# Optimization experiments

Hardware: AMD Instinct MI355X
Metric: run time of the kernel (lower is better)

Reference implementation:

```python
import jax, jax.numpy as jnp
import numpy as np

DIM = 1024
QK_DIM = 128
HIDDEN = 2048  # int(2.0 * DIM)
B, N = 4, 4096


def setup_inputs() -> dict:
    key = jax.random.key(0)
    ks = jax.random.split(key, 10)
    std = 0.02
    return {
        "x": jax.random.normal(ks[0], (B, N, DIM), dtype=jnp.float32),
        "ln_g": jnp.ones((DIM,), jnp.float32),
        "ln_b": jnp.zeros((DIM,), jnp.float32),
        "W_hidden": jax.random.normal(ks[1], (DIM, 2 * HIDDEN), jnp.float32) * (1.0 / np.sqrt(DIM)),
        "b_hidden": jnp.zeros((2 * HIDDEN,), jnp.float32),
        "W_qk": jax.random.normal(ks[2], (DIM, QK_DIM), jnp.float32) * (1.0 / np.sqrt(DIM)),
        "b_qk": jnp.zeros((QK_DIM,), jnp.float32),
        "os_gamma": jax.random.normal(ks[3], (2, QK_DIM), jnp.float32) * std,
        "os_beta": jnp.zeros((2, QK_DIM), jnp.float32),
        "W_out": jax.random.normal(ks[4], (HIDDEN, DIM), jnp.float32) * (1.0 / np.sqrt(HIDDEN)),
        "b_out": jnp.zeros((DIM,), jnp.float32),
    }


def _layernorm(x, g, b, eps=1e-5):
    mu = jnp.mean(x, axis=-1, keepdims=True)
    var = jnp.var(x, axis=-1, keepdims=True)
    return (x - mu) * jax.lax.rsqrt(var + eps) * g + b


def reference(x, ln_g, ln_b, W_hidden, b_hidden, W_qk, b_qk, os_gamma, os_beta, W_out, b_out):
    n = x.shape[-2]
    normed = _layernorm(x, ln_g, ln_b)
    hidden = jax.nn.silu(normed @ W_hidden + b_hidden)  # [b,n,2*hidden]
    v, gate = jnp.split(hidden, 2, axis=-1)             # [b,n,hidden] each
    qk = jax.nn.silu(normed @ W_qk + b_qk)              # [b,n,qk]
    q = qk * os_gamma[0] + os_beta[0]
    k = qk * os_gamma[1] + os_beta[1]
    sim = jnp.einsum('bid,bjd->bij', q, k)
    # causal: divide row i by (i+1)
    denom = (jnp.arange(n, dtype=x.dtype) + 1.0)[:, None]  # [n,1]
    sim = sim / denom
    attn = jnp.square(jax.nn.relu(sim))
    causal_mask = jnp.triu(jnp.ones((n, n), dtype=bool), k=1)
    attn = jnp.where(causal_mask, 0.0, attn)
    out = jnp.einsum('bij,bjd->bid', attn, v)
    out = out * gate
    out = out @ W_out + b_out
    return out + x
```

## Files before the change

### kernel.cpp

```cpp
#include <hip/hip_runtime.h>
#include <hip/hip_bf16.h>
#include <stdint.h>

typedef __bf16 bf16_t;
typedef __bf16 bf16x4 __attribute__((ext_vector_type(4)));
typedef __bf16 bf16x8 __attribute__((ext_vector_type(8)));
typedef float  f32x4  __attribute__((ext_vector_type(4)));
typedef long long i64;

#define MFMA16(a, b, c) __builtin_amdgcn_mfma_f32_16x16x32_bf16((a), (b), (c), 0, 0, 0)
#define MFMAF8(a, b, c) __builtin_amdgcn_mfma_f32_16x16x32_fp8_fp8((a), (b), (c), 0, 0, 0)

static constexpr int TOKS   = 16384;
static constexpr int SEQ    = 4096;
static constexpr int DIMK   = 1024;
static constexpr int H2     = 4096;
static constexpr int HID    = 2048;
static constexpr int QKD    = 128;
static constexpr int SMEM8P = 131072;
static constexpr size_t PBATCH = 8912896;

__device__ __forceinline__ void gload_lds16b(const uint8_t* g, uint8_t* l) {
  __builtin_amdgcn_global_load_lds((__attribute__((address_space(1))) void*)(g),
                                   (__attribute__((address_space(3))) void*)(l),
                                   16, 0, 0);
}

__device__ __forceinline__ float silu_f(float v) { return v / (1.0f + __expf(-v)); }

__device__ __forceinline__ uint32_t f8x4(float a, float b, float c, float d) {
  int v = __builtin_amdgcn_cvt_pk_fp8_f32(a, b, 0, false);
  v = __builtin_amdgcn_cvt_pk_fp8_f32(c, d, v, true);
  return (uint32_t)v;
}
__device__ __forceinline__ uint8_t f8x1(float a) {
  return (uint8_t)(__builtin_amdgcn_cvt_pk_fp8_f32(a, 0.f, 0, false) & 0xff);
}

#define BARRIER() __builtin_amdgcn_s_barrier()

__global__ __launch_bounds__(256) void k_transpose_bf16(const float* __restrict__ W,
                                                        bf16_t* __restrict__ WT,
                                                        int K, int N) {
  __shared__ float t[32][33];
  int n0 = blockIdx.x * 32, k0 = blockIdx.y * 32;
  int tx = threadIdx.x & 31, ty = threadIdx.x >> 5;
#pragma unroll
  for (int r = 0; r < 32; r += 8)
    t[ty + r][tx] = W[(size_t)(k0 + ty + r) * N + n0 + tx];
  __syncthreads();
#pragma unroll
  for (int r = 0; r < 32; r += 8)
    WT[(size_t)(n0 + ty + r) * K + k0 + tx] = (bf16_t)t[tx][ty + r];
}

__global__ __launch_bounds__(256) void k_transpose_f8(const float* __restrict__ W,
                                                      uint8_t* __restrict__ WT,
                                                      int K, int N) {
  __shared__ float t[32][33];
  int n0 = blockIdx.x * 32, k0 = blockIdx.y * 32;
  int tx = threadIdx.x & 31, ty = threadIdx.x >> 5;
#pragma unroll
  for (int r = 0; r < 32; r += 8)
    t[ty + r][tx] = W[(size_t)(k0 + ty + r) * N + n0 + tx];
  __syncthreads();
#pragma unroll
  for (int r = 0; r < 32; r += 8)
    WT[(size_t)(n0 + ty + r) * K + k0 + tx] = f8x1(t[tx][ty + r] * 16.0f);
}

__global__ __launch_bounds__(256) void k_layernorm(const float* __restrict__ x,
                                                   const float* __restrict__ g,
                                                   const float* __restrict__ b,
                                                   bf16_t* __restrict__ out,
                                                   uint8_t* __restrict__ out8) {
  int row = blockIdx.x, t = threadIdx.x;
  const float4* xr = (const float4*)(x + (size_t)row * DIMK);
  float4 v = xr[t];
  float s  = v.x + v.y + v.z + v.w;
  float ss = v.x * v.x + v.y * v.y + v.z * v.z + v.w * v.w;
#pragma unroll
  for (int o = 1; o < 64; o <<= 1) { s += __shfl_xor(s, o); ss += __shfl_xor(ss, o); }
  __shared__ float red[8];
  int wave = t >> 6, lane = t & 63;
  if (lane == 0) { red[wave] = s; red[wave + 4] = ss; }
  __syncthreads();
  s  = red[0] + red[1] + red[2] + red[3];
  ss = red[4] + red[5] + red[6] + red[7];
  float mean = s * (1.0f / DIMK);
  float var  = ss * (1.0f / DIMK) - mean * mean;
  float rstd = rsqrtf(var + 1e-5f);
  float4 gg = ((const float4*)g)[t];
  float4 bb = ((const float4*)b)[t];
  float o0 = (v.x - mean) * rstd * gg.x + bb.x;
  float o1 = (v.y - mean) * rstd * gg.y + bb.y;
  float o2 = (v.z - mean) * rstd * gg.z + bb.z;
  float o3 = (v.w - mean) * rstd * gg.w + bb.w;
  bf16x4 o4; o4[0] = (bf16_t)o0; o4[1] = (bf16_t)o1; o4[2] = (bf16_t)o2; o4[3] = (bf16_t)o3;
  *(bf16x4*)(out + (size_t)row * DIMK + t * 4) = o4;
  *(uint32_t*)(out8 + (size_t)row * DIMK + t * 4) = f8x4(o0, o1, o2, o3);
}

#define MFMAQ8(MH, KP)                                                        \
  _Pragma("unroll")                                                           \
  for (int mi = 0; mi < 4; ++mi)                                              \
    _Pragma("unroll")                                                         \
    for (int nj = 0; nj < 4; ++nj)                                            \
      _Pragma("unroll")                                                       \
      for (int ks = 0; ks < 2; ++ks)                                          \
        acc[(MH) * 4 + mi][nj] = MFMAF8(aF[(MH) * 4 + mi][KP][ks],            \
                                        bF[nj][KP][ks], acc[(MH) * 4 + mi][nj]);

#define RDA8(MILO, KP, BUFO)                                                  \
  _Pragma("unroll")                                                           \
  for (int mi = (MILO); mi < (MILO) + 4; ++mi)                                \
    _Pragma("unroll")                                                         \
    for (int ks = 0; ks < 2; ++ks)                                            \
      aF[mi][KP][ks] = *(const i64*)(pA + (BUFO) + mi * 2048 + swzK[(KP) * 2 + ks]);

#define RDB8(KP, BUFO)                                                        \
  _Pragma("unroll")                                                           \
  for (int nj = 0; nj < 4; ++nj)                                              \
    _Pragma("unroll")                                                         \
    for (int ks = 0; ks < 2; ++ks)                                            \
      bF[nj][KP][ks] = *(const i64*)(pB + (BUFO) + nj * 2048 + swzK[(KP) * 2 + ks]);

__device__ __forceinline__ void core8p_f8(const uint8_t* __restrict__ Ag, int lda,
                                          const uint8_t* __restrict__ Bg, int ldb,
                                          int NK, uint8_t* AS, uint8_t* BS,
                                          f32x4 (&acc)[8][4]) {
  const int tid = threadIdx.x, wid = tid >> 6, lane = tid & 63;
  const int wm = wid >> 2, wn = wid & 3;

  auto stA = [&](int kt, int h) {
    int r0 = h * 128 + wid * 16 + (lane >> 3);
    int c0 = ((lane & 7) ^ ((r0 >> 1) & 7)) * 16;
    uint8_t* d = AS + ((kt & 1) * 2 + h) * 16384 + wid * 2048;
    gload_lds16b(Ag + (size_t)r0 * lda + kt * 128 + c0, d);
    int r1 = r0 + 8;
    int c1 = ((lane & 7) ^ ((r1 >> 1) & 7)) * 16;
    gload_lds16b(Ag + (size_t)r1 * lda + kt * 128 + c1, d + 1024);
  };
  auto stB = [&](int kt, int h) {
    int r0 = h * 128 + wid * 16 + (lane >> 3);
    int c0 = ((lane & 7) ^ ((r0 >> 1) & 7)) * 16;
    uint8_t* d = BS + ((kt & 1) * 2 + h) * 16384 + wid * 2048;
    gload_lds16b(Bg + (size_t)r0 * ldb + kt * 128 + c0, d);
    int r1 = r0 + 8;
    int c1 = ((lane & 7) ^ ((r1 >> 1) & 7)) * 16;
    gload_lds16b(Bg + (size_t)r1 * ldb + kt * 128 + c1, d + 1024);
  };

  int swzK[4];
#pragma unroll
  for (int j = 0; j < 4; ++j)
    swzK[j] = ((j * 4 + (lane >> 4)) ^ (lane & 14)) * 8;

  const uint8_t* pA = AS + wm * 16384 + (lane & 15) * 128;
  const uint8_t* pB = BS + (wn >> 1) * 16384 + ((wn & 1) * 64 + (lane & 15)) * 128;

  i64 aF[8][2][2], bF[4][2][2];

  stA(0, 0); stA(0, 1); stB(0, 0); stB(0, 1);
  stB(1, 0); stB(1, 1);
  asm volatile("s_waitcnt vmcnt(4)" ::: "memory");
  BARRIER();
  RDA8(0, 0, 0);
  RDB8(0, 0);

  for (int g = 0; g < NK; ++g) {
    const int buf  = (g & 1) * 32768;
    const int nbuf = ((g + 1) & 1) * 32768;
    RDA8(4, 0, buf);
    if (g + 1 < NK) stA(g + 1, 0);
    BARRIER();
    __builtin_amdgcn_s_setprio(1);
    MFMAQ8(0, 0);
    __builtin_amdgcn_s_setprio(0);
    RDA8(0, 1, buf);
    RDB8(1, buf);
    if (g + 1 < NK) stA(g + 1, 1);
    BARRIER();
    __builtin_amdgcn_s_setprio(1);
    MFMAQ8(1, 0);
    __builtin_amdgcn_s_setprio(0);
    RDA8(4, 1, buf);
    BARRIER();
    __builtin_amdgcn_s_setprio(1);
    MFMAQ8(0, 1);
    __builtin_amdgcn_s_setprio(0);
    if (g + 2 < NK) {
      stB(g + 2, 0); stB(g + 2, 1);
      asm volatile("s_waitcnt vmcnt(4)" ::: "memory");
    } else if (g + 1 < NK) {
      asm volatile("s_waitcnt vmcnt(0)" ::: "memory");
    }
    BARRIER();
    if (g + 1 < NK) {
      RDA8(0, 0, nbuf);
      RDB8(0, nbuf);
    }
    __builtin_amdgcn_s_setprio(1);
    MFMAQ8(1, 1);
    __builtin_amdgcn_s_setprio(0);
  }
}

__global__ __launch_bounds__(512, 2) void k_gemm_hidden8p(const uint8_t* __restrict__ A,
                                                          const uint8_t* __restrict__ BT,
                                                          const float* __restrict__ bias,
                                                          uint8_t* __restrict__ vT8,
                                                          bf16_t* __restrict__ gate) {
  extern __shared__ __align__(16) uint8_t lds[];
  uint8_t* AS = lds;
  uint8_t* BS = lds + 65536;
  const int nwg = gridDim.x, bid = blockIdx.x;
  const int swz = (bid & 7) * (nwg >> 3) + (bid >> 3);
  const int mblk = swz >> 4, nblk = swz & 15;
  const int m0 = mblk * 256, n0 = nblk * 256;
  f32x4 acc[8][4];
#pragma unroll
  for (int i = 0; i < 8; ++i)
#pragma unroll
    for (int j = 0; j < 4; ++j) acc[i][j] = (f32x4){0.f, 0.f, 0.f, 0.f};
  core8p_f8(A + (size_t)m0 * DIMK, DIMK, BT + (size_t)n0 * DIMK, DIMK,
            DIMK / 128, AS, BS, acc);

  const int tid = threadIdx.x, wid = tid >> 6, lane = tid & 63;
  const int wm = wid >> 2, wn = wid & 3;
  const int row0 = m0 + wm * 128, col0 = n0 + wn * 64;
#pragma unroll
  for (int mi = 0; mi < 8; ++mi)
#pragma unroll
    for (int nj = 0; nj < 4; ++nj) {
      int col = col0 + nj * 16 + (lane & 15);
      float bv = bias[col];
      int row = row0 + mi * 16 + ((lane >> 4) << 2);
      float sv[4];
#pragma unroll
      for (int r = 0; r < 4; ++r) sv[r] = silu_f(acc[mi][nj][r] * 0.0625f + bv);
      if (col < HID) {
        *(uint32_t*)(vT8 + (size_t)col * TOKS + row) =
            f8x4(sv[0] * 16.f, sv[1] * 16.f, sv[2] * 16.f, sv[3] * 16.f);
      } else {
#pragma unroll
        for (int r = 0; r < 4; ++r)
          gate[(size_t)(row + r) * HID + (col - HID)] = (bf16_t)sv[r];
      }
    }
}

__global__ __launch_bounds__(512, 2) void k_gemm_out8p(const uint8_t* __restrict__ A,
                                                       const uint8_t* __restrict__ BT,
                                                       const float* __restrict__ bo,
                                                       const float* __restrict__ x,
                                                       float* __restrict__ out) {
  extern __shared__ __align__(16) uint8_t lds[];
  uint8_t* AS = lds;
  uint8_t* BS = lds + 65536;
  const int nwg = gridDim.x, bid = blockIdx.x;
  const int swz = (bid & 7) * (nwg >> 3) + (bid >> 3);
  const int mblk = swz >> 2, nblk = swz & 3;
  const int m0 = mblk * 256, n0 = nblk * 256;
  f32x4 acc[8][4];
#pragma unroll
  for (int i = 0; i < 8; ++i)
#pragma unroll
    for (int j = 0; j < 4; ++j) acc[i][j] = (f32x4){0.f, 0.f, 0.f, 0.f};
  core8p_f8(A + (size_t)m0 * HID, HID, BT + (size_t)n0 * HID, HID,
            HID / 128, AS, BS, acc);

  const int tid = threadIdx.x, wid = tid >> 6, lane = tid & 63;
  const int wm = wid >> 2, wn = wid & 3;
  const int row0 = m0 + wm * 128, col0 = n0 + wn * 64;
#pragma unroll
  for (int mi = 0; mi < 8; ++mi)
#pragma unroll
    for (int nj = 0; nj < 4; ++nj) {
      int col = col0 + nj * 16 + (lane & 15);
      float bv = bo[col];
      int row = row0 + mi * 16 + ((lane >> 4) << 2);
#pragma unroll
      for (int r = 0; r < 4; ++r) {
        size_t gi = (size_t)(row + r) * DIMK + col;
        out[gi] = acc[mi][nj][r] * (1.0f / 4096.0f) + bv + x[gi];
      }
    }
}

__global__ __launch_bounds__(512, 2) void k_pv8p(const uint8_t* __restrict__ P8,
                                                 const uint8_t* __restrict__ vT8,
                                                 const bf16_t* __restrict__ gate,
                                                 uint8_t* __restrict__ gated8) {
  extern __shared__ __align__(16) uint8_t lds[];
  uint8_t* AS = lds;
  uint8_t* BS = lds + 65536;
  const int w = blockIdx.x;
  const int rb = 15 - (w >> 5);
  const int hb = (w >> 2) & 7;
  const int bb = w & 3;
  const int lda = (rb + 1) * 256;
  const uint8_t* Ag = P8 + (size_t)bb * PBATCH + (size_t)65536 * (rb * (rb + 1) / 2);
  const uint8_t* Bg = vT8 + (size_t)(hb * 256) * TOKS + (size_t)bb * SEQ;
  f32x4 acc[8][4];
#pragma unroll
  for (int i = 0; i < 8; ++i)
#pragma unroll
    for (int j = 0; j < 4; ++j) acc[i][j] = (f32x4){0.f, 0.f, 0.f, 0.f};
  core8p_f8(Ag, lda, Bg, TOKS, (rb + 1) * 2, AS, BS, acc);

  const int tid = threadIdx.x, wid = tid >> 6, lane = tid & 63;
  const int wm = wid >> 2, wn = wid & 3;
  const int row0 = rb * 256 + wm * 128, col0 = hb * 256 + wn * 64;
#pragma unroll
  for (int mi = 0; mi < 8; ++mi)
#pragma unroll
    for (int nj = 0; nj < 4; ++nj) {
      int col = col0 + nj * 16 + (lane & 15);
      int row = row0 + mi * 16 + ((lane >> 4) << 2);
#pragma unroll
      for (int r = 0; r < 4; ++r) {
        size_t gi = (size_t)(bb * SEQ + row + r) * HID + col;
        float gv = (float)gate[gi];
        gated8[gi] = f8x1(acc[mi][nj][r] * gv * 6.103515625e-05f);
      }
    }
}

__device__ __forceinline__ void gload_lds16(const bf16_t* g, bf16_t* l) {
  __builtin_amdgcn_global_load_lds((__attribute__((address_space(1))) void*)(g),
                                   (__attribute__((address_space(3))) void*)(l),
                                   16, 0, 0);
}

__device__ __forceinline__ void gemm_core_std(const bf16_t* __restrict__ Ag0, int lda,
                                              const bf16_t* __restrict__ Bg0, int ldb,
                                              int K, bf16_t* As, bf16_t* Bs,
                                              f32x4 acc[4][4]) {
  const int tid = threadIdx.x;
  const int wave = tid >> 6, lane = tid & 63;
  bf16_t* asw = As + wave * 32 * 32;
  bf16_t* bsw = Bs + wave * 32 * 32;
  const int ar = ((wave >> 1) * 64 + (lane & 15)) * 32 + (lane >> 4) * 8;
  const int br = ((wave & 1) * 64 + (lane & 15)) * 32 + (lane >> 4) * 8;
  for (int k0 = 0; k0 < K; k0 += 32) {
    __syncthreads();
    gload_lds16(Ag0 + k0, asw);
    gload_lds16(Ag0 + k0 + 16 * lda, asw + 16 * 32);
    gload_lds16(Bg0 + k0, bsw);
    gload_lds16(Bg0 + k0 + 16 * ldb, bsw + 16 * 32);
    __syncthreads();
    bf16x8 af[4], bfr[4];
#pragma unroll
    for (int m = 0; m < 4; m++) af[m] = *(const bf16x8*)(As + ar + m * 16 * 32);
#pragma unroll
    for (int n = 0; n < 4; n++) bfr[n] = *(const bf16x8*)(Bs + br + n * 16 * 32);
#pragma unroll
    for (int m = 0; m < 4; m++)
#pragma unroll
      for (int n = 0; n < 4; n++) acc[m][n] = MFMA16(af[m], bfr[n], acc[m][n]);
  }
}

__global__ __launch_bounds__(256) void k_gemm_qk(const bf16_t* __restrict__ A,
                                                 const bf16_t* __restrict__ BT,
                                                 const float* __restrict__ bias,
                                                 const float* __restrict__ osg,
                                                 const float* __restrict__ osb,
                                                 bf16_t* __restrict__ qo,
                                                 bf16_t* __restrict__ ko) {
  __shared__ __align__(16) bf16_t As[128 * 32];
  __shared__ __align__(16) bf16_t Bs[128 * 32];
  const int tid = threadIdx.x, wave = tid >> 6, lane = tid & 63;
  const int m0 = blockIdx.y * 128;
  const bf16_t* Ag0 = A + (size_t)(m0 + wave * 32 + (lane >> 2)) * DIMK + (lane & 3) * 8;
  const bf16_t* Bg0 = BT + (size_t)(wave * 32 + (lane >> 2)) * DIMK + (lane & 3) * 8;
  f32x4 acc[4][4];
#pragma unroll
  for (int m = 0; m < 4; m++)
#pragma unroll
    for (int n = 0; n < 4; n++) acc[m][n] = (f32x4){0.f, 0.f, 0.f, 0.f};
  gemm_core_std(Ag0, DIMK, Bg0, DIMK, DIMK, As, Bs, acc);

  const int row0 = m0 + (wave >> 1) * 64;
  const int col0 = (wave & 1) * 64;
#pragma unroll
  for (int m = 0; m < 4; m++) {
#pragma unroll
    for (int n = 0; n < 4; n++) {
      int col = col0 + n * 16 + (lane & 15);
      float bv = bias[col];
      float g0 = osg[col], b0 = osb[col];
      float g1 = osg[QKD + col], b1 = osb[QKD + col];
      int row = row0 + m * 16 + ((lane >> 4) << 2);
#pragma unroll
      for (int r = 0; r < 4; r++) {
        float sv = silu_f(acc[m][n][r] + bv);
        qo[(size_t)(row + r) * QKD + col] = (bf16_t)(sv * g0 + b0);
        ko[(size_t)(row + r) * QKD + col] = (bf16_t)(sv * g1 + b1);
      }
    }
  }
}

__global__ __launch_bounds__(256) void k_qkt(const bf16_t* __restrict__ qb,
                                             const bf16_t* __restrict__ kb,
                                             uint8_t* __restrict__ P8) {
  const int jb = blockIdx.x, ib = blockIdx.y, bb = blockIdx.z;
  const int rb = ib >> 1;
  if (jb > 2 * rb + 1) return;
  const int lda = (rb + 1) * 256;
  uint8_t* Pt = P8 + (size_t)bb * PBATCH + (size_t)65536 * (rb * (rb + 1) / 2)
              + (size_t)((ib & 1) * 128) * lda + jb * 128;
  if (jb == ib + 1) {
    const int row = threadIdx.x >> 1, cb = (threadIdx.x & 1) * 64;
    uint4 z = {0, 0, 0, 0};
#pragma unroll
    for (int c = 0; c < 64; c += 16)
      *(uint4*)(Pt + (size_t)row * lda + cb + c) = z;
    return;
  }
  __shared__ __align__(16) bf16_t As[128 * 32];
  __shared__ __align__(16) bf16_t Bs[128 * 32];
  const int tid = threadIdx.x, wave = tid >> 6, lane = tid & 63;
  const bf16_t* Ag0 = qb + (size_t)(bb * SEQ + ib * 128 + wave * 32 + (lane >> 2)) * QKD + (lane & 3) * 8;
  const bf16_t* Bg0 = kb + (size_t)(bb * SEQ + jb * 128 + wave * 32 + (lane >> 2)) * QKD + (lane & 3) * 8;
  f32x4 acc[4][4];
#pragma unroll
  for (int m = 0; m < 4; m++)
#pragma unroll
    for (int n = 0; n < 4; n++) acc[m][n] = (f32x4){0.f, 0.f, 0.f, 0.f};
  gemm_core_std(Ag0, QKD, Bg0, QKD, QKD, As, Bs, acc);

  const int il0 = (wave >> 1) * 64, jl0 = (wave & 1) * 64;
#pragma unroll
  for (int m = 0; m < 4; m++) {
#pragma unroll
    for (int n = 0; n < 4; n++) {
      int jloc = jl0 + n * 16 + (lane & 15);
      int jg = jb * 128 + jloc;
#pragma unroll
      for (int r = 0; r < 4; r++) {
        int iloc = il0 + m * 16 + ((lane >> 4) << 2) + r;
        int ig = ib * 128 + iloc;
        float sv = acc[m][n][r] / (float)(ig + 1);
        sv = fmaxf(sv, 0.f);
        sv *= sv;
        if (jg > ig) sv = 0.f;
        Pt[(size_t)iloc * lda + jloc] = f8x1(sv * 262144.0f);
      }
    }
  }
}

extern "C" void kernel_launch(void* const* d_in, const int* in_sizes, int n_in,
                              void* d_out, int out_size, void* d_ws, size_t ws_size,
                              hipStream_t stream) {
  (void)in_sizes; (void)n_in; (void)out_size; (void)ws_size;
  const float* x    = (const float*)d_in[0];
  const float* ln_g = (const float*)d_in[1];
  const float* ln_b = (const float*)d_in[2];
  const float* Wh   = (const float*)d_in[3];
  const float* bh   = (const float*)d_in[4];
  const float* Wqk  = (const float*)d_in[5];
  const float* bqk  = (const float*)d_in[6];
  const float* osg  = (const float*)d_in[7];
  const float* osb  = (const float*)d_in[8];
  const float* Wo   = (const float*)d_in[9];
  const float* bo   = (const float*)d_in[10];
  float* out = (float*)d_out;

  char* ws = (char*)d_ws;
  bf16_t* normed  = (bf16_t*)ws;  ws += (size_t)TOKS * DIMK * 2;
  uint8_t* normed8 = (uint8_t*)ws; ws += (size_t)TOKS * DIMK;
  bf16_t* WqkT    = (bf16_t*)ws;  ws += (size_t)QKD * DIMK * 2;
  uint8_t* Wh8T   = (uint8_t*)ws; ws += (size_t)H2 * DIMK;
  uint8_t* Wo8T   = (uint8_t*)ws; ws += (size_t)DIMK * HID;
  bf16_t* gate    = (bf16_t*)ws;  ws += (size_t)TOKS * HID * 2;
  uint8_t* vT8    = (uint8_t*)ws; ws += (size_t)HID * TOKS;
  uint8_t* gated8 = (uint8_t*)ws; ws += (size_t)TOKS * HID;
  bf16_t* qb      = (bf16_t*)ws;  ws += (size_t)TOKS * QKD * 2;
  bf16_t* kb      = (bf16_t*)ws;  ws += (size_t)TOKS * QKD * 2;
  uint8_t* P8     = (uint8_t*)ws; ws += (size_t)4 * PBATCH;

  hipFuncSetAttribute((const void*)k_gemm_hidden8p,
                      hipFuncAttributeMaxDynamicSharedMemorySize, SMEM8P);
  hipFuncSetAttribute((const void*)k_gemm_out8p,
                      hipFuncAttributeMaxDynamicSharedMemorySize, SMEM8P);
  hipFuncSetAttribute((const void*)k_pv8p,
                      hipFuncAttributeMaxDynamicSharedMemorySize, SMEM8P);

  k_transpose_f8<<<dim3(H2 / 32, DIMK / 32), 256, 0, stream>>>(Wh, Wh8T, DIMK, H2);
  k_transpose_f8<<<dim3(DIMK / 32, HID / 32), 256, 0, stream>>>(Wo, Wo8T, HID, DIMK);
  k_transpose_bf16<<<dim3(QKD / 32, DIMK / 32), 256, 0, stream>>>(Wqk, WqkT, DIMK, QKD);
  k_layernorm<<<TOKS, 256, 0, stream>>>(x, ln_g, ln_b, normed, normed8);
  k_gemm_hidden8p<<<dim3((TOKS / 256) * (H2 / 256)), 512, SMEM8P, stream>>>(normed8, Wh8T, bh, vT8, gate);
  k_gemm_qk<<<dim3(1, TOKS / 128), 256, 0, stream>>>(normed, WqkT, bqk, osg, osb, qb, kb);
  k_qkt<<<dim3(SEQ / 128, SEQ / 128, 4), 256, 0, stream>>>(qb, kb, P8);
  k_pv8p<<<dim3(16 * 8 * 4), 512, SMEM8P, stream>>>(P8, vT8, gate, gated8);
  k_gemm_out8p<<<dim3((TOKS / 256) * (DIMK / 256)), 512, SMEM8P, stream>>>(gated8, Wo8T, bo, x, out);
}
```

Before: 406.8 us.

## Switch FP8 GEMM core to scaled 16x16x128 MFMA with new LDS swizzle

Replaces the four 16x16x32 fp8 MFMAs per K-tile slice with the gfx950 scaled 16x16x128 f8f6f4 MFMA using unit scales. Fragments are now read from LDS as two 16-byte loads per lane, and the swizzle pattern changes to match. The register layout and read schedule are restructured to fit, which cuts the MFMA instruction count and LDS read instructions. It risks K-ordering and layout mismatches between the operands, and a different register pressure profile.

```diff
diff --git a/kernel.cpp b/kernel.cpp
--- a/kernel.cpp
+++ b/kernel.cpp
@@ -6,10 +6,11 @@
 typedef __bf16 bf16x4 __attribute__((ext_vector_type(4)));
 typedef __bf16 bf16x8 __attribute__((ext_vector_type(8)));
 typedef float  f32x4  __attribute__((ext_vector_type(4)));
-typedef long long i64;
+typedef int    i32x8  __attribute__((ext_vector_type(8)));
 
 #define MFMA16(a, b, c) __builtin_amdgcn_mfma_f32_16x16x32_bf16((a), (b), (c), 0, 0, 0)
-#define MFMAF8(a, b, c) __builtin_amdgcn_mfma_f32_16x16x32_fp8_fp8((a), (b), (c), 0, 0, 0)
+#define MFMAMX(a, b, c) \
+  __builtin_amdgcn_mfma_scale_f32_16x16x128_f8f6f4((a), (b), (c), 0, 0, 0, 127, 0, 127)
 
 static constexpr int TOKS   = 16384;
 static constexpr int SEQ    = 4096;
@@ -35,6 +36,12 @@
 }
 __device__ __forceinline__ uint8_t f8x1(float a) {
   return (uint8_t)(__builtin_amdgcn_cvt_pk_fp8_f32(a, 0.f, 0, false) & 0xff);
+}
+
+__device__ __forceinline__ i32x8 rd32(const uint8_t* p0, const uint8_t* p1) {
+  const int4 lo = *(const int4*)p0;
+  const int4 hi = *(const int4*)p1;
+  return (i32x8){lo.x, lo.y, lo.z, lo.w, hi.x, hi.y, hi.z, hi.w};
 }
 
 #define BARRIER() __builtin_amdgcn_s_barrier()
@@ -101,29 +108,22 @@
   *(uint32_t*)(out8 + (size_t)row * DIMK + t * 4) = f8x4(o0, o1, o2, o3);
 }
 
-#define MFMAQ8(MH, KP)                                                        \
+#define RDAF(MILO, BUFO)                                                      \
   _Pragma("unroll")                                                           \
-  for (int mi = 0; mi < 4; ++mi)                                              \
+  for (int mi = (MILO); mi < (MILO) + 2; ++mi)                                \
+    aF[mi] = rd32(pA + (BUFO) + mi * 2048 + sw0, pA + (BUFO) + mi * 2048 + sw1);
+
+#define RDBF(BUFO)                                                            \
+  _Pragma("unroll")                                                           \
+  for (int nj = 0; nj < 4; ++nj)                                              \
+    bF[nj] = rd32(pB + (BUFO) + nj * 2048 + sw0, pB + (BUFO) + nj * 2048 + sw1);
+
+#define MFMAQX(Q)                                                             \
+  _Pragma("unroll")                                                           \
+  for (int mi = (Q) * 2; mi < (Q) * 2 + 2; ++mi)                              \
     _Pragma("unroll")                                                         \
     for (int nj = 0; nj < 4; ++nj)                                            \
-      _Pragma("unroll")                                                       \
-      for (int ks = 0; ks < 2; ++ks)                                          \
-        acc[(MH) * 4 + mi][nj] = MFMAF8(aF[(MH) * 4 + mi][KP][ks],            \
-                                        bF[nj][KP][ks], acc[(MH) * 4 + mi][nj]);
-
-#define RDA8(MILO, KP, BUFO)                                                  \
-  _Pragma("unroll")                                                           \
-  for (int mi = (MILO); mi < (MILO) + 4; ++mi)                                \
-    _Pragma("unroll")                                                         \
-    for (int ks = 0; ks < 2; ++ks)                                            \
-      aF[mi][KP][ks] = *(const i64*)(pA + (BUFO) + mi * 2048 + swzK[(KP) * 2 + ks]);
-
-#define RDB8(KP, BUFO)                                                        \
-  _Pragma("unroll")                                                           \
-  for (int nj = 0; nj < 4; ++nj)                                              \
-    _Pragma("unroll")                                                         \
-    for (int ks = 0; ks < 2; ++ks)                                            \
-      bF[nj][KP][ks] = *(const i64*)(pB + (BUFO) + nj * 2048 + swzK[(KP) * 2 + ks]);
+      acc[mi][nj] = MFMAMX(aF[mi], bF[nj], acc[mi][nj]);
 
 __device__ __forceinline__ void core8p_f8(const uint8_t* __restrict__ Ag, int lda,
                                           const uint8_t* __restrict__ Bg, int ldb,
@@ -134,60 +134,54 @@
 
   auto stA = [&](int kt, int h) {
     int r0 = h * 128 + wid * 16 + (lane >> 3);
-    int c0 = ((lane & 7) ^ ((r0 >> 1) & 7)) * 16;
+    int c0 = ((lane & 7) ^ ((lane >> 3) & 7)) * 16;
     uint8_t* d = AS + ((kt & 1) * 2 + h) * 16384 + wid * 2048;
     gload_lds16b(Ag + (size_t)r0 * lda + kt * 128 + c0, d);
-    int r1 = r0 + 8;
-    int c1 = ((lane & 7) ^ ((r1 >> 1) & 7)) * 16;
-    gload_lds16b(Ag + (size_t)r1 * lda + kt * 128 + c1, d + 1024);
+    gload_lds16b(Ag + (size_t)(r0 + 8) * lda + kt * 128 + c0, d + 1024);
   };
   auto stB = [&](int kt, int h) {
     int r0 = h * 128 + wid * 16 + (lane >> 3);
-    int c0 = ((lane & 7) ^ ((r0 >> 1) & 7)) * 16;
+    int c0 = ((lane & 7) ^ ((lane >> 3) & 7)) * 16;
     uint8_t* d = BS + ((kt & 1) * 2 + h) * 16384 + wid * 2048;
     gload_lds16b(Bg + (size_t)r0 * ldb + kt * 128 + c0, d);
-    int r1 = r0 + 8;
-    int c1 = ((lane & 7) ^ ((r1 >> 1) & 7)) * 16;
-    gload_lds16b(Bg + (size_t)r1 * ldb + kt * 128 + c1, d + 1024);
+    gload_lds16b(Bg + (size_t)(r0 + 8) * ldb + kt * 128 + c0, d + 1024);
   };
 
-  int swzK[4];
-#pragma unroll
-  for (int j = 0; j < 4; ++j)
-    swzK[j] = ((j * 4 + (lane >> 4)) ^ (lane & 14)) * 8;
+  const int t = lane >> 4;
+  const int sw0 = ((2 * t) ^ (lane & 7)) * 16;
+  const int sw1 = ((2 * t + 1) ^ (lane & 7)) * 16;
 
   const uint8_t* pA = AS + wm * 16384 + (lane & 15) * 128;
   const uint8_t* pB = BS + (wn >> 1) * 16384 + ((wn & 1) * 64 + (lane & 15)) * 128;
 
-  i64 aF[8][2][2], bF[4][2][2];
+  i32x8 aF[8], bF[4];
 
   stA(0, 0); stA(0, 1); stB(0, 0); stB(0, 1);
   stB(1, 0); stB(1, 1);
   asm volatile("s_waitcnt vmcnt(4)" ::: "memory");
   BARRIER();
-  RDA8(0, 0, 0);
-  RDB8(0, 0);
+  RDAF(0, 0);
+  RDBF(0);
 
   for (int g = 0; g < NK; ++g) {
     const int buf  = (g & 1) * 32768;
     const int nbuf = ((g + 1) & 1) * 32768;
-    RDA8(4, 0, buf);
+    RDAF(2, buf);
     if (g + 1 < NK) stA(g + 1, 0);
     BARRIER();
     __builtin_amdgcn_s_setprio(1);
-    MFMAQ8(0, 0);
+    MFMAQX(0);
     __builtin_amdgcn_s_setprio(0);
-    RDA8(0, 1, buf);
-    RDB8(1, buf);
+    RDAF(4, buf);
     if (g + 1 < NK) stA(g + 1, 1);
     BARRIER();
     __builtin_amdgcn_s_setprio(1);
-    MFMAQ8(1, 0);
+    MFMAQX(1);
     __builtin_amdgcn_s_setprio(0);
-    RDA8(4, 1, buf);
+    RDAF(6, buf);
     BARRIER();
     __builtin_amdgcn_s_setprio(1);
-    MFMAQ8(0, 1);
+    MFMAQX(2);
     __builtin_amdgcn_s_setprio(0);
     if (g + 2 < NK) {
       stB(g + 2, 0); stB(g + 2, 1);
@@ -197,11 +191,11 @@
     }
     BARRIER();
     if (g + 1 < NK) {
-      RDA8(0, 0, nbuf);
-      RDB8(0, nbuf);
+      RDAF(0, nbuf);
+      RDBF(nbuf);
     }
     __builtin_amdgcn_s_setprio(1);
-    MFMAQ8(1, 1);
+    MFMAQX(3);
     __builtin_amdgcn_s_setprio(0);
   }
 }
```

Result: slower. 1.455 ms (+257.6%).

## Permute fp8 K-dimension layout so MFMA operands load as 128-bit LDS reads

Applied to the files above, without the earlier changes.

All fp8 producers (weight transpose, layernorm, vT, gated, P) now write each 128-wide K chunk in a permuted order. In that order, the two 8-byte fragments a lane needs for consecutive MFMA k-steps sit next to each other. The fp8 GEMM core then reads each fragment pair with one 16-byte LDS load instead of two 8-byte loads, and the row-dependent swizzle is simplified. This halves the number of LDS read instructions in the core, at the cost of scattered byte-level stores in the epilogues and more index arithmetic.

```diff
diff --git a/kernel.cpp b/kernel.cpp
--- a/kernel.cpp
+++ b/kernel.cpp
@@ -7,6 +7,7 @@
 typedef __bf16 bf16x8 __attribute__((ext_vector_type(8)));
 typedef float  f32x4  __attribute__((ext_vector_type(4)));
 typedef long long i64;
+typedef long long i64x2 __attribute__((ext_vector_type(2)));
 
 #define MFMA16(a, b, c) __builtin_amdgcn_mfma_f32_16x16x32_bf16((a), (b), (c), 0, 0, 0)
 #define MFMAF8(a, b, c) __builtin_amdgcn_mfma_f32_16x16x32_fp8_fp8((a), (b), (c), 0, 0, 0)
@@ -37,6 +38,11 @@
   return (uint8_t)(__builtin_amdgcn_cvt_pk_fp8_f32(a, 0.f, 0, false) & 0xff);
 }
 
+__device__ __forceinline__ int permk(int kb) {
+  int b = kb & 7, t = (kb >> 3) & 3, s = (kb >> 5) & 1, a = (kb >> 6) & 1;
+  return (a << 6) | (t << 4) | (s << 3) | b;
+}
+
 #define BARRIER() __builtin_amdgcn_s_barrier()
 
 __global__ __launch_bounds__(256) void k_transpose_bf16(const float* __restrict__ W,
@@ -65,8 +71,11 @@
     t[ty + r][tx] = W[(size_t)(k0 + ty + r) * N + n0 + tx];
   __syncthreads();
 #pragma unroll
-  for (int r = 0; r < 32; r += 8)
-    WT[(size_t)(n0 + ty + r) * K + k0 + tx] = f8x1(t[tx][ty + r] * 16.0f);
+  for (int r = 0; r < 32; r += 8) {
+    int kt = k0 + tx;
+    WT[(size_t)(n0 + ty + r) * K + (kt & ~127) + permk(kt & 127)] =
+        f8x1(t[tx][ty + r] * 16.0f);
+  }
 }
 
 __global__ __launch_bounds__(256) void k_layernorm(const float* __restrict__ x,
@@ -98,7 +107,9 @@
   float o3 = (v.w - mean) * rstd * gg.w + bb.w;
   bf16x4 o4; o4[0] = (bf16_t)o0; o4[1] = (bf16_t)o1; o4[2] = (bf16_t)o2; o4[3] = (bf16_t)o3;
   *(bf16x4*)(out + (size_t)row * DIMK + t * 4) = o4;
-  *(uint32_t*)(out8 + (size_t)row * DIMK + t * 4) = f8x4(o0, o1, o2, o3);
+  int kt = t * 4;
+  *(uint32_t*)(out8 + (size_t)row * DIMK + (kt & ~127) + permk(kt & 127)) =
+      f8x4(o0, o1, o2, o3);
 }
 
 #define MFMAQ8(MH, KP)                                                        \
@@ -114,16 +125,12 @@
 #define RDA8(MILO, KP, BUFO)                                                  \
   _Pragma("unroll")                                                           \
   for (int mi = (MILO); mi < (MILO) + 4; ++mi)                                \
-    _Pragma("unroll")                                                         \
-    for (int ks = 0; ks < 2; ++ks)                                            \
-      aF[mi][KP][ks] = *(const i64*)(pA + (BUFO) + mi * 2048 + swzK[(KP) * 2 + ks]);
+    aF[mi][KP] = *(const i64x2*)(pA + (BUFO) + mi * 2048 + swc[KP]);
 
 #define RDB8(KP, BUFO)                                                        \
   _Pragma("unroll")                                                           \
   for (int nj = 0; nj < 4; ++nj)                                              \
-    _Pragma("unroll")                                                         \
-    for (int ks = 0; ks < 2; ++ks)                                            \
-      bF[nj][KP][ks] = *(const i64*)(pB + (BUFO) + nj * 2048 + swzK[(KP) * 2 + ks]);
+    bF[nj][KP] = *(const i64x2*)(pB + (BUFO) + nj * 2048 + swc[KP]);
 
 __device__ __forceinline__ void core8p_f8(const uint8_t* __restrict__ Ag, int lda,
                                           const uint8_t* __restrict__ Bg, int ldb,
@@ -131,35 +138,31 @@
                                           f32x4 (&acc)[8][4]) {
   const int tid = threadIdx.x, wid = tid >> 6, lane = tid & 63;
   const int wm = wid >> 2, wn = wid & 3;
+  const int srow = lane >> 3;
+  const int scol = ((lane & 7) ^ srow) * 16;
 
   auto stA = [&](int kt, int h) {
-    int r0 = h * 128 + wid * 16 + (lane >> 3);
-    int c0 = ((lane & 7) ^ ((r0 >> 1) & 7)) * 16;
+    int r0 = h * 128 + wid * 16 + srow;
     uint8_t* d = AS + ((kt & 1) * 2 + h) * 16384 + wid * 2048;
-    gload_lds16b(Ag + (size_t)r0 * lda + kt * 128 + c0, d);
-    int r1 = r0 + 8;
-    int c1 = ((lane & 7) ^ ((r1 >> 1) & 7)) * 16;
-    gload_lds16b(Ag + (size_t)r1 * lda + kt * 128 + c1, d + 1024);
+    gload_lds16b(Ag + (size_t)r0 * lda + kt * 128 + scol, d);
+    gload_lds16b(Ag + (size_t)(r0 + 8) * lda + kt * 128 + scol, d + 1024);
   };
   auto stB = [&](int kt, int h) {
-    int r0 = h * 128 + wid * 16 + (lane >> 3);
-    int c0 = ((lane & 7) ^ ((r0 >> 1) & 7)) * 16;
+    int r0 = h * 128 + wid * 16 + srow;
     uint8_t* d = BS + ((kt & 1) * 2 + h) * 16384 + wid * 2048;
-    gload_lds16b(Bg + (size_t)r0 * ldb + kt * 128 + c0, d);
-    int r1 = r0 + 8;
-    int c1 = ((lane & 7) ^ ((r1 >> 1) & 7)) * 16;
-    gload_lds16b(Bg + (size_t)r1 * ldb + kt * 128 + c1, d + 1024);
+    gload_lds16b(Bg + (size_t)r0 * ldb + kt * 128 + scol, d);
+    gload_lds16b(Bg + (size_t)(r0 + 8) * ldb + kt * 128 + scol, d + 1024);
   };
 
-  int swzK[4];
-#pragma unroll
-  for (int j = 0; j < 4; ++j)
-    swzK[j] = ((j * 4 + (lane >> 4)) ^ (lane & 14)) * 8;
+  const int t = lane >> 4;
+  int swc[2];
+  swc[0] = ((0 * 4 + t) ^ (lane & 7)) * 16;
+  swc[1] = ((1 * 4 + t) ^ (lane & 7)) * 16;
 
   const uint8_t* pA = AS + wm * 16384 + (lane & 15) * 128;
   const uint8_t* pB = BS + (wn >> 1) * 16384 + ((wn & 1) * 64 + (lane & 15)) * 128;
 
-  i64 aF[8][2][2], bF[4][2][2];
+  i64x2 aF[8][2], bF[4][2];
 
   stA(0, 0); stA(0, 1); stB(0, 0); stB(0, 1);
   stB(1, 0); stB(1, 1);
@@ -240,7 +243,7 @@
 #pragma unroll
       for (int r = 0; r < 4; ++r) sv[r] = silu_f(acc[mi][nj][r] * 0.0625f + bv);
       if (col < HID) {
-        *(uint32_t*)(vT8 + (size_t)col * TOKS + row) =
+        *(uint32_t*)(vT8 + (size_t)col * TOKS + (row & ~127) + permk(row & 127)) =
             f8x4(sv[0] * 16.f, sv[1] * 16.f, sv[2] * 16.f, sv[3] * 16.f);
       } else {
 #pragma unroll
@@ -317,12 +320,13 @@
 #pragma unroll
     for (int nj = 0; nj < 4; ++nj) {
       int col = col0 + nj * 16 + (lane & 15);
-      int row = row0 + mi * 16 + ((lane >> 4) << 2);
+      int pcol = (col & ~127) | permk(col & 127);
 #pragma unroll
       for (int r = 0; r < 4; ++r) {
-        size_t gi = (size_t)(bb * SEQ + row + r) * HID + col;
-        float gv = (float)gate[gi];
-        gated8[gi] = f8x1(acc[mi][nj][r] * gv * 6.103515625e-05f);
+        int row = row0 + mi * 16 + ((lane >> 4) << 2) + r;
+        size_t tok = (size_t)(bb * SEQ + row);
+        float gv = (float)gate[tok * HID + col];
+        gated8[tok * HID + pcol] = f8x1(acc[mi][nj][r] * gv * 6.103515625e-05f);
       }
     }
 }
@@ -439,6 +443,7 @@
     for (int n = 0; n < 4; n++) {
       int jloc = jl0 + n * 16 + (lane & 15);
       int jg = jb * 128 + jloc;
+      int jp = permk(jloc);
 #pragma unroll
       for (int r = 0; r < 4; r++) {
         int iloc = il0 + m * 16 + ((lane >> 4) << 2) + r;
@@ -447,7 +452,7 @@
         sv = fmaxf(sv, 0.f);
         sv *= sv;
         if (jg > ig) sv = 0.f;
-        Pt[(size_t)iloc * lda + jloc] = f8x1(sv * 262144.0f);
+        Pt[(size_t)iloc * lda + jp] = f8x1(sv * 262144.0f);
       }
     }
   }
```

Result: faster. 390.2 us (median of 2 runs) (-4.1%).
